# Kernel optimization log

Measured on AMD Instinct MI355X. Metric: run time of the kernel, lower is better.

Reference implementation:

```python
import jax, jax.numpy as jnp
import numpy as np

B, S, D = 8, 1024, 1024   # batch, routed-over rows, feature dim (input_dim)
E = 1024                  # output_dim (== S so gather indices are in range)
K = 2                     # top-k
ALPHA = 0.01


def setup_inputs() -> dict:
    key = jax.random.key(0)
    kx, kw = jax.random.split(key)
    x = jax.random.normal(kx, (B, S, D), dtype=jnp.float32)
    # nn.Linear(input_dim, output_dim, bias=False) weight: [E, D]
    W = jax.random.normal(kw, (E, D), dtype=jnp.float32) / np.sqrt(D).astype(np.float32)
    return {"x": x, "W": W}


def reference(x, W):
    # logits = proj(x): [B, S, E]  (temperature == 1.0 -> no scaling)
    logits = jnp.einsum('bsd,ed->bse', x, W)
    probs = jax.nn.softmax(logits, axis=-1)
    topk_probs, topk_idx = jax.lax.top_k(probs, K)            # [B, S, K]
    # router_selections: gather rows of x along dim 1 -> [B, S, K, D]
    sel = x[jnp.arange(B)[:, None, None], topk_idx]
    # y = sum_k topk_probs * selected rows -> [B, S, D]
    y = jnp.einsum('bsk,bskd->bsd', topk_probs, sel)
    # auxiliary load-balance loss
    router_probs = probs.mean(axis=(0, 1))                    # [E]
    counts = jnp.bincount(topk_idx.reshape(-1), length=E).astype(probs.dtype)
    router_fraction = counts / counts.sum()
    aux_loss = ALPHA * E * jnp.sum(router_probs * router_fraction)
    return y, aux_loss
```

## Files before the change

kernel.cpp:

```cpp
#include <hip/hip_runtime.h>

#define MTOK 8192
#define ED   1024

typedef short s16x8 __attribute__((ext_vector_type(8)));
typedef float f32x4 __attribute__((ext_vector_type(4)));
typedef unsigned short u16x4 __attribute__((ext_vector_type(4)));

__device__ __forceinline__ unsigned short f2bf(float f) {
    unsigned u = __builtin_bit_cast(unsigned, f);
    u += 0x7fff + ((u >> 16) & 1);
    return (unsigned short)(u >> 16);
}
__device__ __forceinline__ float bf2f(unsigned short h) {
    unsigned u = ((unsigned)h) << 16;
    return __builtin_bit_cast(float, u);
}

__global__ __launch_bounds__(256) void split_bf16_kernel(
        const float* __restrict__ src, unsigned short* __restrict__ hi,
        unsigned short* __restrict__ lo, int n4) {
    int idx = blockIdx.x * 256 + threadIdx.x;
    const int stride = gridDim.x * 256;
    for (; idx < n4; idx += stride) {
        float4 v = ((const float4*)src)[idx];
        u16x4 h, l;
        h[0] = f2bf(v.x); l[0] = f2bf(v.x - bf2f(h[0]));
        h[1] = f2bf(v.y); l[1] = f2bf(v.y - bf2f(h[1]));
        h[2] = f2bf(v.z); l[2] = f2bf(v.z - bf2f(h[2]));
        h[3] = f2bf(v.w); l[3] = f2bf(v.w - bf2f(h[3]));
        ((u16x4*)hi)[idx] = h;
        ((u16x4*)lo)[idx] = l;
    }
}

__device__ __forceinline__ void gload16(const void* g, void* l) {
    __builtin_amdgcn_global_load_lds(
        (const __attribute__((address_space(1))) void*)g,
        (__attribute__((address_space(3))) void*)l, 16, 0, 0);
}

__global__ __launch_bounds__(256, 2) void gemm_mfma_split_kernel(
        const unsigned short* __restrict__ Xhi, const unsigned short* __restrict__ Xlo,
        const unsigned short* __restrict__ Whi, const unsigned short* __restrict__ Wlo,
        float* __restrict__ C) {
    __shared__ unsigned short smem[4 * 4096];
    unsigned short* const Ahi = smem;
    unsigned short* const Alo = smem + 4096;
    unsigned short* const Bhi = smem + 8192;
    unsigned short* const Blo = smem + 12288;

    const int bid = blockIdx.x;
    const int lin = (bid & 7) * 64 + (bid >> 3);
    const int bn = lin >> 6;
    const int bm = lin & 63;

    const int tid  = threadIdx.x;
    const int lane = tid & 63;
    const int wid  = tid >> 6;

    const int srow = lane >> 2;
    const int sg   = (lane & 3) ^ ((srow >> 1) & 3);
    const unsigned short* gsrc;
    unsigned short* ldst;
    {
        size_t rb;
        if (wid == 0)      { gsrc = Xhi; ldst = Ahi; rb = (size_t)bm * 128; }
        else if (wid == 1) { gsrc = Xlo; ldst = Alo; rb = (size_t)bm * 128; }
        else if (wid == 2) { gsrc = Whi; ldst = Bhi; rb = (size_t)bn * 128; }
        else               { gsrc = Wlo; ldst = Blo; rb = (size_t)bn * 128; }
        gsrc += (rb + srow) * ED + sg * 8;
    }

    const int wm = wid >> 1, wn = wid & 1;
    const int fr = lane & 15, fg = lane >> 4;
    const int pg = fg ^ ((fr >> 1) & 3);
    const int aoff = (wm * 64 + fr) * 32 + pg * 8;
    const int boff = (wn * 64 + fr) * 32 + pg * 8;

    f32x4 acc[4][4] = {};

    for (int k0 = 0; k0 < ED; k0 += 32) {
        __syncthreads();
#pragma unroll
        for (int c = 0; c < 8; ++c)
            gload16(gsrc + k0 + c * (16 * ED), ldst + c * 512);
        __syncthreads();

        s16x8 ah[4], al[4], bh[4], bl[4];
#pragma unroll
        for (int i = 0; i < 4; ++i) {
            ah[i] = *(const s16x8*)&Ahi[aoff + i * 512];
            al[i] = *(const s16x8*)&Alo[aoff + i * 512];
            bh[i] = *(const s16x8*)&Bhi[boff + i * 512];
            bl[i] = *(const s16x8*)&Blo[boff + i * 512];
        }
#pragma unroll
        for (int i = 0; i < 4; ++i)
#pragma unroll
            for (int j = 0; j < 4; ++j) {
                acc[i][j] = __builtin_amdgcn_mfma_f32_16x16x32_bf16(ah[i], bh[j], acc[i][j], 0, 0, 0);
                acc[i][j] = __builtin_amdgcn_mfma_f32_16x16x32_bf16(ah[i], bl[j], acc[i][j], 0, 0, 0);
                acc[i][j] = __builtin_amdgcn_mfma_f32_16x16x32_bf16(al[i], bh[j], acc[i][j], 0, 0, 0);
            }
    }

    const int crow = bm * 128 + wm * 64 + fg * 4;
    const int ccol = bn * 128 + wn * 64 + fr;
#pragma unroll
    for (int i = 0; i < 4; ++i)
#pragma unroll
        for (int j = 0; j < 4; ++j)
#pragma unroll
            for (int r = 0; r < 4; ++r)
                C[(size_t)(crow + i * 16 + r) * ED + ccol + j * 16] = acc[i][j][r];
}

#define BM 128
#define BN 128
#define BK 32
#define LDA (BM + 4)
#define LDB (BN + 4)

__global__ __launch_bounds__(256) void gemm_logits_kernel(const float* __restrict__ X,
                                                          const float* __restrict__ W,
                                                          float* __restrict__ C) {
    __shared__ float As[BK][LDA];
    __shared__ float Bs[BK][LDB];
    const int bm  = blockIdx.y * BM;
    const int bn  = blockIdx.x * BN;
    const int tid = threadIdx.x;
    const int tx  = tid & 15;
    const int ty  = tid >> 4;
    const int lr  = tid >> 3;
    const int lc  = (tid & 7) << 2;

    float acc[8][8];
#pragma unroll
    for (int i = 0; i < 8; ++i)
#pragma unroll
        for (int j = 0; j < 8; ++j) acc[i][j] = 0.f;

    for (int k0 = 0; k0 < ED; k0 += BK) {
#pragma unroll
        for (int i = 0; i < 4; ++i) {
            const int r = lr + i * 32;
            float4 va = *(const float4*)&X[(size_t)(bm + r) * ED + k0 + lc];
            As[lc + 0][r] = va.x; As[lc + 1][r] = va.y;
            As[lc + 2][r] = va.z; As[lc + 3][r] = va.w;
            float4 vb = *(const float4*)&W[(size_t)(bn + r) * ED + k0 + lc];
            Bs[lc + 0][r] = vb.x; Bs[lc + 1][r] = vb.y;
            Bs[lc + 2][r] = vb.z; Bs[lc + 3][r] = vb.w;
        }
        __syncthreads();
#pragma unroll
        for (int kk = 0; kk < BK; ++kk) {
            float a[8], b[8];
            *(float4*)&a[0] = *(const float4*)&As[kk][ty * 8];
            *(float4*)&a[4] = *(const float4*)&As[kk][ty * 8 + 4];
            *(float4*)&b[0] = *(const float4*)&Bs[kk][tx * 8];
            *(float4*)&b[4] = *(const float4*)&Bs[kk][tx * 8 + 4];
#pragma unroll
            for (int i = 0; i < 8; ++i)
#pragma unroll
                for (int j = 0; j < 8; ++j)
                    acc[i][j] = fmaf(a[i], b[j], acc[i][j]);
        }
        __syncthreads();
    }
#pragma unroll
    for (int i = 0; i < 8; ++i) {
        const int r = bm + ty * 8 + i;
        float4* dst = (float4*)&C[(size_t)r * ED + bn + tx * 8];
        dst[0] = make_float4(acc[i][0], acc[i][1], acc[i][2], acc[i][3]);
        dst[1] = make_float4(acc[i][4], acc[i][5], acc[i][6], acc[i][7]);
    }
}

__device__ __forceinline__ bool better(float v, int i, float bv, int bi) {
    return (v > bv) || (v == bv && i < bi);
}

__global__ __launch_bounds__(256, 8) void softmax_wave_kernel(
        const float* __restrict__ X, float* __restrict__ OUT,
        float* __restrict__ partial, int* __restrict__ counts) {
    __shared__ float L[4 * 1024];
    const int tid  = threadIdx.x;
    const int lane = tid & 63;
    const int w    = tid >> 6;
    const int t    = blockIdx.x * 4 + w;

    const float4* row4 = (const float4*)&OUT[(size_t)t * ED];
    float4 p[4];
#pragma unroll
    for (int i = 0; i < 4; ++i) p[i] = row4[lane + 64 * i];

    float v1 = -1e30f, v2 = -1e30f; int i1 = 0x7fffffff, i2 = 0x7fffffff;
#pragma unroll
    for (int i = 0; i < 4; ++i) {
        const float vv[4] = {p[i].x, p[i].y, p[i].z, p[i].w};
#pragma unroll
        for (int c = 0; c < 4; ++c) {
            const int e = 256 * i + 4 * lane + c;
            const float v = vv[c];
            if (better(v, e, v1, i1)) { v2 = v1; i2 = i1; v1 = v; i1 = e; }
            else if (better(v, e, v2, i2)) { v2 = v; i2 = e; }
        }
    }
#pragma unroll
    for (int off = 32; off; off >>= 1) {
        const float ov1 = __shfl_xor(v1, off); const int oi1 = __shfl_xor(i1, off);
        const float ov2 = __shfl_xor(v2, off); const int oi2 = __shfl_xor(i2, off);
        if (better(ov1, oi1, v1, i1)) {
            float nv2; int ni2;
            if (better(v1, i1, ov2, oi2)) { nv2 = v1; ni2 = i1; }
            else { nv2 = ov2; ni2 = oi2; }
            v1 = ov1; i1 = oi1; v2 = nv2; i2 = ni2;
        } else if (better(ov1, oi1, v2, i2)) { v2 = ov1; i2 = oi1; }
    }
    const float m = v1;

    float s = 0.f;
#pragma unroll
    for (int i = 0; i < 4; ++i) {
        p[i].x = __expf(p[i].x - m); p[i].y = __expf(p[i].y - m);
        p[i].z = __expf(p[i].z - m); p[i].w = __expf(p[i].w - m);
        s += p[i].x + p[i].y + p[i].z + p[i].w;
    }
#pragma unroll
    for (int off = 32; off; off >>= 1) s += __shfl_xor(s, off);
    const float inv = 1.f / s;

#pragma unroll
    for (int i = 0; i < 4; ++i) {
        float4 q = make_float4(p[i].x * inv, p[i].y * inv, p[i].z * inv, p[i].w * inv);
        *(float4*)&L[w * 1024 + i * 256 + lane * 4] = q;
    }

    const float p1 = inv;
    const float p2 = __expf(v2 - m) * inv;
    const int b = t >> 10;
    const float4* x1 = (const float4*)&X[((size_t)(b << 10) + i1) * ED];
    const float4* x2 = (const float4*)&X[((size_t)(b << 10) + i2) * ED];
    float4* yrow = (float4*)&OUT[(size_t)t * ED];
#pragma unroll
    for (int i = 0; i < 4; ++i) {
        const int idx = lane + 64 * i;
        const float4 a = x1[idx];
        const float4 c = x2[idx];
        float4 r;
        r.x = fmaf(p1, a.x, p2 * c.x);
        r.y = fmaf(p1, a.y, p2 * c.y);
        r.z = fmaf(p1, a.z, p2 * c.z);
        r.w = fmaf(p1, a.w, p2 * c.w);
        yrow[idx] = r;
    }

    if (lane == 0) { atomicAdd(&counts[i1], 1); atomicAdd(&counts[i2], 1); }

    __syncthreads();
    float4 s0 = *(float4*)&L[0 * 1024 + tid * 4];
    float4 s1 = *(float4*)&L[1 * 1024 + tid * 4];
    float4 s2 = *(float4*)&L[2 * 1024 + tid * 4];
    float4 s3 = *(float4*)&L[3 * 1024 + tid * 4];
    float4 r;
    r.x = (s0.x + s1.x) + (s2.x + s3.x);
    r.y = (s0.y + s1.y) + (s2.y + s3.y);
    r.z = (s0.z + s1.z) + (s2.z + s3.z);
    r.w = (s0.w + s1.w) + (s2.w + s3.w);
    *(float4*)&partial[(size_t)blockIdx.x * 1024 + tid * 4] = r;
}

__global__ __launch_bounds__(256) void aux1_kernel(const float* __restrict__ partial,
                                                   const int* __restrict__ counts,
                                                   float* __restrict__ dotPartial) {
    __shared__ float red[16][16];
    const int tid = threadIdx.x;
    const int el  = tid & 15;
    const int ch  = tid >> 4;
    const int e   = blockIdx.x * 16 + el;
    float s = 0.f;
    for (int k = 0; k < 128; ++k)
        s += partial[(size_t)(ch * 128 + k) * 1024 + e];
    red[ch][el] = s;
    __syncthreads();
    if (tid < 16) {
        float rs = 0.f;
#pragma unroll
        for (int c = 0; c < 16; ++c) rs += red[c][tid];
        float val = rs * (float)counts[blockIdx.x * 16 + tid];
#pragma unroll
        for (int off = 8; off; off >>= 1) val += __shfl_xor(val, off);
        if (tid == 0) dotPartial[blockIdx.x] = val;
    }
}

__global__ void aux2_kernel(const float* __restrict__ dotPartial, float* __restrict__ out) {
    const int lane = threadIdx.x;
    float v = dotPartial[lane];
#pragma unroll
    for (int off = 32; off; off >>= 1) v += __shfl_xor(v, off);
    if (lane == 0)
        out[(size_t)MTOK * ED] = v * (0.01f * 1024.f / (8192.f * 16384.f));
}

#define TOKS_PER_BLK 16
__global__ __launch_bounds__(256) void softmax_topk_y_kernel(
        const float* __restrict__ X, float* __restrict__ OUT,
        float* __restrict__ router_sum, int* __restrict__ counts) {
    __shared__ float routerLocal[ED];
    __shared__ float redMax[4];
    __shared__ float redSum[4];
    __shared__ float wV1[4]; __shared__ int wI1[4];
    __shared__ float wV2[4]; __shared__ int wI2[4];

    const int tid  = threadIdx.x;
    const int lane = tid & 63;
    const int wave = tid >> 6;

    for (int e = tid; e < ED; e += 256) routerLocal[e] = 0.f;
    __syncthreads();

    const int t0 = blockIdx.x * TOKS_PER_BLK;
    for (int t = t0; t < t0 + TOKS_PER_BLK; ++t) {
        const float* lrow = &OUT[(size_t)t * ED];
        float l[4];
#pragma unroll
        for (int i = 0; i < 4; ++i) l[i] = lrow[tid + i * 256];

        float m = fmaxf(fmaxf(l[0], l[1]), fmaxf(l[2], l[3]));
#pragma unroll
        for (int off = 32; off; off >>= 1) m = fmaxf(m, __shfl_xor(m, off));
        if (lane == 0) redMax[wave] = m;
        __syncthreads();
        m = fmaxf(fmaxf(redMax[0], redMax[1]), fmaxf(redMax[2], redMax[3]));

        float p[4]; float s = 0.f;
#pragma unroll
        for (int i = 0; i < 4; ++i) { p[i] = expf(l[i] - m); s += p[i]; }
#pragma unroll
        for (int off = 32; off; off >>= 1) s += __shfl_xor(s, off);
        if (lane == 0) redSum[wave] = s;

        float v1 = -1e30f, v2 = -1e30f; int i1 = 0x7fffffff, i2 = 0x7fffffff;
#pragma unroll
        for (int i = 0; i < 4; ++i) {
            const float v = l[i]; const int ix = tid + i * 256;
            if (better(v, ix, v1, i1)) { v2 = v1; i2 = i1; v1 = v; i1 = ix; }
            else if (better(v, ix, v2, i2)) { v2 = v; i2 = ix; }
        }
#pragma unroll
        for (int off = 32; off; off >>= 1) {
            const float ov1 = __shfl_xor(v1, off); const int oi1 = __shfl_xor(i1, off);
            const float ov2 = __shfl_xor(v2, off); const int oi2 = __shfl_xor(i2, off);
            if (better(ov1, oi1, v1, i1)) {
                float nv2; int ni2;
                if (better(v1, i1, ov2, oi2)) { nv2 = v1; ni2 = i1; }
                else { nv2 = ov2; ni2 = oi2; }
                v1 = ov1; i1 = oi1; v2 = nv2; i2 = ni2;
            } else if (better(ov1, oi1, v2, i2)) { v2 = ov1; i2 = oi1; }
        }
        if (lane == 0) { wV1[wave] = v1; wI1[wave] = i1; wV2[wave] = v2; wI2[wave] = i2; }
        __syncthreads();

        v1 = wV1[0]; i1 = wI1[0]; v2 = wV2[0]; i2 = wI2[0];
#pragma unroll
        for (int w = 1; w < 4; ++w) {
            const float ov1 = wV1[w]; const int oi1 = wI1[w];
            const float ov2 = wV2[w]; const int oi2 = wI2[w];
            if (better(ov1, oi1, v1, i1)) {
                float nv2; int ni2;
                if (better(v1, i1, ov2, oi2)) { nv2 = v1; ni2 = i1; }
                else { nv2 = ov2; ni2 = oi2; }
                v1 = ov1; i1 = oi1; v2 = nv2; i2 = ni2;
            } else if (better(ov1, oi1, v2, i2)) { v2 = ov1; i2 = oi1; }
        }
        const float stot = redSum[0] + redSum[1] + redSum[2] + redSum[3];
        const float inv = 1.f / stot;

#pragma unroll
        for (int i = 0; i < 4; ++i) routerLocal[tid + i * 256] += p[i] * inv;

        const float p1 = expf(v1 - m) * inv;
        const float p2 = expf(v2 - m) * inv;

        const int b = t >> 10;
        const float4* x1 = (const float4*)&X[((size_t)(b << 10) + i1) * ED];
        const float4* x2 = (const float4*)&X[((size_t)(b << 10) + i2) * ED];
        float4* yrow = (float4*)&OUT[(size_t)t * ED];
        const float4 a = x1[tid];
        const float4 c = x2[tid];
        float4 r;
        r.x = fmaf(p1, a.x, p2 * c.x);
        r.y = fmaf(p1, a.y, p2 * c.y);
        r.z = fmaf(p1, a.z, p2 * c.z);
        r.w = fmaf(p1, a.w, p2 * c.w);
        yrow[tid] = r;

        if (tid == 0) { atomicAdd(&counts[i1], 1); atomicAdd(&counts[i2], 1); }
        __syncthreads();
    }

    for (int e = tid; e < ED; e += 256) atomicAdd(&router_sum[e], routerLocal[e]);
}

__global__ __launch_bounds__(256) void aux_kernel(const float* __restrict__ router_sum,
                                                  const int* __restrict__ counts,
                                                  float* __restrict__ out) {
    __shared__ float red[4];
    const int tid = threadIdx.x;
    float s = 0.f;
    for (int e = tid; e < ED; e += 256)
        s += (router_sum[e] * (1.f / 8192.f)) * ((float)counts[e] * (1.f / 16384.f));
#pragma unroll
    for (int off = 32; off; off >>= 1) s += __shfl_xor(s, off);
    if ((tid & 63) == 0) red[tid >> 6] = s;
    __syncthreads();
    if (tid == 0) out[(size_t)MTOK * ED] = 0.01f * 1024.f * (red[0] + red[1] + red[2] + red[3]);
}

extern "C" void kernel_launch(void* const* d_in, const int* in_sizes, int n_in,
                              void* d_out, int out_size, void* d_ws, size_t ws_size,
                              hipStream_t stream) {
    const float* X = (const float*)d_in[0];
    const float* W = (const float*)d_in[1];
    float* out = (float*)d_out;

    const size_t WS_NEED = (size_t)MTOK * ED * 2 * sizeof(unsigned short)
                         + (size_t)ED * ED * 2 * sizeof(unsigned short)
                         + ED * (sizeof(float) + sizeof(int));

    if (ws_size >= WS_NEED) {
        unsigned short* Xhi = (unsigned short*)d_ws;
        unsigned short* Xlo = Xhi + (size_t)MTOK * ED;
        unsigned short* Whi = Xlo + (size_t)MTOK * ED;
        unsigned short* Wlo = Whi + (size_t)ED * ED;
        float* tail         = (float*)(Wlo + (size_t)ED * ED);
        float* dotPartial   = tail;
        int*   counts       = (int*)(tail + ED);
        float* partial      = (float*)Xlo;

        hipMemsetAsync(counts, 0, ED * sizeof(int), stream);
        split_bf16_kernel<<<2048, 256, 0, stream>>>(X, Xhi, Xlo, MTOK * ED / 4);
        split_bf16_kernel<<<512, 256, 0, stream>>>(W, Whi, Wlo, ED * ED / 4);
        gemm_mfma_split_kernel<<<512, 256, 0, stream>>>(Xhi, Xlo, Whi, Wlo, out);
        softmax_wave_kernel<<<MTOK / 4, 256, 0, stream>>>(X, out, partial, counts);
        aux1_kernel<<<64, 256, 0, stream>>>(partial, counts, dotPartial);
        aux2_kernel<<<1, 64, 0, stream>>>(dotPartial, out);
    } else {
        float* router_sum = (float*)d_ws;
        int*   counts     = (int*)((char*)d_ws + ED * sizeof(float));
        hipMemsetAsync(d_ws, 0, ED * (sizeof(float) + sizeof(int)), stream);
        dim3 ggrid(ED / BN, MTOK / BM);
        gemm_logits_kernel<<<ggrid, 256, 0, stream>>>(X, W, out);
        softmax_topk_y_kernel<<<MTOK / TOKS_PER_BLK, 256, 0, stream>>>(X, out, router_sum, counts);
        aux_kernel<<<1, 256, 0, stream>>>(router_sum, counts, out);
    }
}
```

Before: 106.4 us.

## Double-buffer LDS tiles in split-bf16 MFMA GEMM and remap XCD block order

Doubles shared memory to two stage buffers so the next K tile's global-to-LDS loads are issued before the MFMAs on the current tile, with one waitcnt plus barrier per iteration instead of two syncthreads. The block-to-tile mapping also changes so each XCD handles a contiguous band of row tiles across all column tiles, aiming for better L2 reuse of X. LDS use doubles to 64KB per block, which may limit occupancy under launch_bounds(256,2).

```diff
diff --git a/kernel.cpp b/kernel.cpp
--- a/kernel.cpp
+++ b/kernel.cpp
@@ -44,16 +44,13 @@
         const unsigned short* __restrict__ Xhi, const unsigned short* __restrict__ Xlo,
         const unsigned short* __restrict__ Whi, const unsigned short* __restrict__ Wlo,
         float* __restrict__ C) {
-    __shared__ unsigned short smem[4 * 4096];
-    unsigned short* const Ahi = smem;
-    unsigned short* const Alo = smem + 4096;
-    unsigned short* const Bhi = smem + 8192;
-    unsigned short* const Blo = smem + 12288;
+    __shared__ unsigned short smem[2 * 16384];
 
     const int bid = blockIdx.x;
-    const int lin = (bid & 7) * 64 + (bid >> 3);
-    const int bn = lin >> 6;
-    const int bm = lin & 63;
+    const int xcd = bid & 7;
+    const int j   = bid >> 3;
+    const int bm  = xcd * 8 + (j >> 3);
+    const int bn  = j & 7;
 
     const int tid  = threadIdx.x;
     const int lane = tid & 63;
@@ -65,11 +62,20 @@
     unsigned short* ldst;
     {
         size_t rb;
-        if (wid == 0)      { gsrc = Xhi; ldst = Ahi; rb = (size_t)bm * 128; }
-        else if (wid == 1) { gsrc = Xlo; ldst = Alo; rb = (size_t)bm * 128; }
-        else if (wid == 2) { gsrc = Whi; ldst = Bhi; rb = (size_t)bn * 128; }
-        else               { gsrc = Wlo; ldst = Blo; rb = (size_t)bn * 128; }
+        if (wid == 0)      { gsrc = Xhi; ldst = smem;         rb = (size_t)bm * 128; }
+        else if (wid == 1) { gsrc = Xlo; ldst = smem + 4096;  rb = (size_t)bm * 128; }
+        else if (wid == 2) { gsrc = Whi; ldst = smem + 8192;  rb = (size_t)bn * 128; }
+        else               { gsrc = Wlo; ldst = smem + 12288; rb = (size_t)bn * 128; }
         gsrc += (rb + srow) * ED + sg * 8;
+    }
+
+#define STAGE(buf, kk)                                                        \
+    {                                                                          \
+        unsigned short* dst = ldst + (buf) * 16384;                            \
+        const unsigned short* src = gsrc + (kk);                               \
+        _Pragma("unroll")                                                      \
+        for (int c = 0; c < 8; ++c)                                            \
+            gload16(src + c * (16 * ED), dst + c * 512);                       \
     }
 
     const int wm = wid >> 1, wn = wid & 1;
@@ -80,40 +86,50 @@
 
     f32x4 acc[4][4] = {};
 
-    for (int k0 = 0; k0 < ED; k0 += 32) {
-        __syncthreads();
-#pragma unroll
-        for (int c = 0; c < 8; ++c)
-            gload16(gsrc + k0 + c * (16 * ED), ldst + c * 512);
-        __syncthreads();
+    STAGE(0, 0);
+    asm volatile("s_waitcnt vmcnt(0)" ::: "memory");
+    __builtin_amdgcn_s_barrier();
+
+    for (int t = 0; t < 32; ++t) {
+        const int cur = t & 1;
+        if (t < 31) STAGE(cur ^ 1, (t + 1) * 32);
+
+        const unsigned short* Ah = smem + cur * 16384;
+        const unsigned short* Al = Ah + 4096;
+        const unsigned short* Bh = Ah + 8192;
+        const unsigned short* Bl = Ah + 12288;
 
         s16x8 ah[4], al[4], bh[4], bl[4];
 #pragma unroll
         for (int i = 0; i < 4; ++i) {
-            ah[i] = *(const s16x8*)&Ahi[aoff + i * 512];
-            al[i] = *(const s16x8*)&Alo[aoff + i * 512];
-            bh[i] = *(const s16x8*)&Bhi[boff + i * 512];
-            bl[i] = *(const s16x8*)&Blo[boff + i * 512];
+            ah[i] = *(const s16x8*)&Ah[aoff + i * 512];
+            al[i] = *(const s16x8*)&Al[aoff + i * 512];
+            bh[i] = *(const s16x8*)&Bh[boff + i * 512];
+            bl[i] = *(const s16x8*)&Bl[boff + i * 512];
         }
 #pragma unroll
         for (int i = 0; i < 4; ++i)
 #pragma unroll
-            for (int j = 0; j < 4; ++j) {
-                acc[i][j] = __builtin_amdgcn_mfma_f32_16x16x32_bf16(ah[i], bh[j], acc[i][j], 0, 0, 0);
-                acc[i][j] = __builtin_amdgcn_mfma_f32_16x16x32_bf16(ah[i], bl[j], acc[i][j], 0, 0, 0);
-                acc[i][j] = __builtin_amdgcn_mfma_f32_16x16x32_bf16(al[i], bh[j], acc[i][j], 0, 0, 0);
+            for (int jj = 0; jj < 4; ++jj) {
+                acc[i][jj] = __builtin_amdgcn_mfma_f32_16x16x32_bf16(ah[i], bh[jj], acc[i][jj], 0, 0, 0);
+                acc[i][jj] = __builtin_amdgcn_mfma_f32_16x16x32_bf16(ah[i], bl[jj], acc[i][jj], 0, 0, 0);
+                acc[i][jj] = __builtin_amdgcn_mfma_f32_16x16x32_bf16(al[i], bh[jj], acc[i][jj], 0, 0, 0);
             }
-    }
+
+        asm volatile("s_waitcnt vmcnt(0)" ::: "memory");
+        __builtin_amdgcn_s_barrier();
+    }
+#undef STAGE
 
     const int crow = bm * 128 + wm * 64 + fg * 4;
     const int ccol = bn * 128 + wn * 64 + fr;
 #pragma unroll
     for (int i = 0; i < 4; ++i)
 #pragma unroll
-        for (int j = 0; j < 4; ++j)
+        for (int jj = 0; jj < 4; ++jj)
 #pragma unroll
             for (int r = 0; r < 4; ++r)
-                C[(size_t)(crow + i * 16 + r) * ED + ccol + j * 16] = acc[i][j][r];
+                C[(size_t)(crow + i * 16 + r) * ED + ccol + jj * 16] = acc[i][jj][r];
 }
 
 #define BM 128
```

Result: faster. 101.2 us (-4.9%).
